# Performance work log

Hardware: AMD Instinct MI355X
Metric: run time of the kernel (lower is better)

The kernel has to match this reference:

```python
import jax, jax.numpy as jnp
import numpy as np

B, L, D, H = 2, 2048, 1024, 16
HD = D // H


def setup_inputs() -> dict:
    key = jax.random.key(0)
    ks = jax.random.split(key, 12)
    s = 1.0 / np.sqrt(D)
    inp = {
        "q": jax.random.normal(ks[0], (B, L, D), jnp.float32),
        "k": jax.random.normal(ks[1], (B, L, D), jnp.float32),
        "v": jax.random.normal(ks[2], (B, L, D), jnp.float32),
        "mask": jnp.zeros((B, L), dtype=bool),  # True = masked out
        "Wq": jax.random.normal(ks[3], (D, D), jnp.float32) * s,
        "bq": jnp.zeros((D,), jnp.float32),
        "Wk": jax.random.normal(ks[4], (D, D), jnp.float32) * s,
        "bk": jnp.zeros((D,), jnp.float32),
        "Wv": jax.random.normal(ks[5], (D, D), jnp.float32) * s,
        "bv": jnp.zeros((D,), jnp.float32),
        "Wo": jax.random.normal(ks[6], (D, D), jnp.float32) * s,
        "bo": jnp.zeros((D,), jnp.float32),
    }
    return inp


def reference(q, k, v, mask, Wq, bq, Wk, bk, Wv, bv, Wo, bo):
    # linear projections (torch Linear: x @ W.T + b), split into heads: [B,H,L,HD]
    def proj(x, W, b):
        y = jnp.einsum('bld,ed->ble', x, W) + b
        return y.reshape(x.shape[0], x.shape[1], H, HD).transpose(0, 2, 1, 3)

    Q = proj(q, Wq, bq)
    K = proj(k, Wk, bk)
    V = proj(v, Wv, bv)

    scale = 1.0 / np.sqrt(HD).astype(np.float32)
    scores = jnp.einsum('bhqd,bhkd->bhqk', Q, K) * scale  # [B,H,Lq,Lk]
    # mask [B,Lk] -> broadcast over heads and query positions
    scores = jnp.where(mask[:, None, None, :], -jnp.inf, scores)
    attn = jax.nn.softmax(scores, axis=-1)
    out = jnp.einsum('bhqk,bhkd->bhqd', attn, V)  # [B,H,Lq,HD]
    out = out.transpose(0, 2, 1, 3).reshape(q.shape[0], q.shape[1], D)
    return jnp.einsum('bld,ed->ble', out, Wo) + bo
```

## Files before the change

kernel.cpp:

```cpp
#include <hip/hip_runtime.h>

#define LSEQ 2048
#define DMODEL 1024
#define NHEAD 16
#define HDIM 64

typedef __attribute__((ext_vector_type(8))) short bf16x8;
typedef __attribute__((ext_vector_type(4))) float f32x4;
typedef __attribute__((ext_vector_type(16))) float f32x16;
typedef unsigned int u32;
typedef unsigned short u16;
typedef unsigned long long u64;

static __device__ __forceinline__ u16 f2bf(float x) {
    return (u16)((__builtin_bit_cast(u32, x) + 0x8000u) >> 16);
}

static __device__ __forceinline__ u32 f2bf_pk(float hi, float lo) {
    u32 a = __builtin_bit_cast(u32, hi) + 0x8000u;
    u32 b = __builtin_bit_cast(u32, lo) + 0x8000u;
#if __has_builtin(__builtin_amdgcn_perm)
    return __builtin_amdgcn_perm(a, b, 0x07060302u);
#else
    return (a & 0xFFFF0000u) | (b >> 16);
#endif
}

static __device__ __forceinline__ float bf2f(short s) {
    return __builtin_bit_cast(float, (u32)((u16)s) << 16);
}

static __device__ __forceinline__ float fast_exp2(float x) {
#if __has_builtin(__builtin_amdgcn_exp2f)
    return __builtin_amdgcn_exp2f(x);
#else
    return __expf(x * 0.6931471805599453f);
#endif
}

static __device__ __forceinline__ void gll16(const void* g, void* l) {
    __builtin_amdgcn_global_load_lds(
        (const __attribute__((address_space(1))) u32*)g,
        (__attribute__((address_space(3))) u32*)l, 16, 0, 0);
}

template <int N>
static __device__ __forceinline__ void vwait() {
    asm volatile("s_waitcnt vmcnt(%0)" :: "n"(N) : "memory");
}

__global__ __launch_bounds__(256) void conv_all(
    const float* __restrict__ q, const float* __restrict__ k, const float* __restrict__ v,
    const float* __restrict__ w0, const float* __restrict__ w1,
    const float* __restrict__ w2, const float* __restrict__ w3,
    u16* __restrict__ Qf, u16* __restrict__ Kf, u16* __restrict__ Vf,
    u16* __restrict__ o0, u16* __restrict__ o1, u16* __restrict__ o2,
    u16* __restrict__ o3) {
    const int bid = blockIdx.x;
    const float* s; u16* d; int off;
    if (bid < 12288) {
        const int z = bid >> 12;
        off = bid & 4095;
        if (z == 0)      { s = q; d = Qf; }
        else if (z == 1) { s = k; d = Kf; }
        else             { s = v; d = Vf; }
    } else {
        const int t = bid - 12288;
        const int z = t >> 10;
        off = t & 1023;
        if (z == 0)      { s = w0; d = o0; }
        else if (z == 1) { s = w1; d = o1; }
        else if (z == 2) { s = w2; d = o2; }
        else             { s = w3; d = o3; }
    }
    const int i = (off * 256 + threadIdx.x) * 4;
    float4 x = *(const float4*)(s + i);
    uint2 r;
    r.x = f2bf_pk(x.y, x.x);
    r.y = f2bf_pk(x.w, x.z);
    *(uint2*)(d + i) = r;
}

template <int OUT_MODE, int BN>
__device__ __forceinline__ void mfma_gemm(u16* __restrict__ sm,
                                          const u16* __restrict__ Xb,
                                          const u16* __restrict__ Wb,
                                          const float* __restrict__ bias,
                                          void* __restrict__ Yv, float scale) {
    constexpr int NB = BN / 32;
    constexpr int LPT = (BN == 128) ? 4 : 3;
    constexpr int ASZ = 4096;
    constexpr int BSZ = BN * 32;
    constexpr int NT = DMODEL / 32;
    u16* As = sm;
    u16* Bs = sm + 3 * ASZ;

    const int tid = threadIdx.x;
    const int wave = tid >> 6, lane = tid & 63;
    const int l16 = lane & 15, quad = lane >> 4;
    const int wm = (wave >> 1) * 64, wn = (wave & 1) * (BN / 2);
    const int m0 = blockIdx.x * 128, n0 = blockIdx.y * BN;

    const u16* Xr = Xb + (size_t)(m0 + (tid >> 2)) * DMODEL + (tid & 3) * 8;
    const u16* Wr = Wb + (size_t)(n0 + (tid >> 2)) * DMODEL + (tid & 3) * 8;
    const int t8 = tid * 8;

    auto stage = [&](int kt, int slot) {
        const int k0 = kt * 32;
        u16* Ab = As + slot * ASZ;
        u16* Bb = Bs + slot * BSZ;
        gll16(Xr + k0, Ab + t8);
        gll16(Xr + (size_t)64 * DMODEL + k0, Ab + 2048 + t8);
        gll16(Wr + k0, Bb + t8);
        if (BN == 128)
            gll16(Wr + (size_t)64 * DMODEL + k0, Bb + 2048 + t8);
    };

    f32x4 acc[4][NB];
    #pragma unroll
    for (int i = 0; i < 4; ++i)
        #pragma unroll
        for (int j = 0; j < NB; ++j)
            #pragma unroll
            for (int r = 0; r < 4; ++r) acc[i][j][r] = 0.0f;

    auto compute = [&](int kt) {
        const u16* Ac = As + (kt % 3) * ASZ;
        const u16* Bc = Bs + (kt % 3) * BSZ;
        bf16x8 af[4], bf[NB];
        #pragma unroll
        for (int mb = 0; mb < 4; ++mb)
            af[mb] = *(const bf16x8*)(Ac + (wm + mb * 16 + l16) * 32 + quad * 8);
        #pragma unroll
        for (int nb = 0; nb < NB; ++nb)
            bf[nb] = *(const bf16x8*)(Bc + (wn + nb * 16 + l16) * 32 + quad * 8);
        #pragma unroll
        for (int mb = 0; mb < 4; ++mb)
            #pragma unroll
            for (int nb = 0; nb < NB; ++nb)
                acc[mb][nb] = __builtin_amdgcn_mfma_f32_16x16x32_bf16(
                    af[mb], bf[nb], acc[mb][nb], 0, 0, 0);
    };

    stage(0, 0);
    stage(1, 1);

    #pragma unroll 1
    for (int kt = 0; kt < NT - 1; ++kt) {
        vwait<LPT>();
        __builtin_amdgcn_s_barrier();
        if (kt + 2 < NT) stage(kt + 2, (kt + 2) % 3);
        compute(kt);
    }
    vwait<0>();
    __builtin_amdgcn_s_barrier();
    compute(NT - 1);

    #pragma unroll
    for (int nb = 0; nb < NB; ++nb) {
        const int n = n0 + wn + nb * 16 + l16;
        const float bn = bias[n];
        #pragma unroll
        for (int mb = 0; mb < 4; ++mb) {
            const int mb0 = m0 + wm + mb * 16 + quad * 4;
            if (OUT_MODE == 2) {
                u16* Y = (u16*)Yv;
                uint2 rr;
                rr.x = f2bf_pk((acc[mb][nb][1] + bn) * scale, (acc[mb][nb][0] + bn) * scale);
                rr.y = f2bf_pk((acc[mb][nb][3] + bn) * scale, (acc[mb][nb][2] + bn) * scale);
                const int bb = mb0 >> 11, l = mb0 & 2047;
                const int h = n >> 6, hd = n & 63;
                *(uint2*)(Y + ((size_t)((bb * NHEAD + h) * HDIM) + hd) * LSEQ + l) = rr;
            } else {
                #pragma unroll
                for (int r = 0; r < 4; ++r) {
                    const int m = mb0 + r;
                    const float val = (acc[mb][nb][r] + bn) * scale;
                    if (OUT_MODE == 0) {
                        u16* Y = (u16*)Yv;
                        const int bb = m >> 11, l = m & 2047;
                        const int h = n >> 6, hd = n & 63;
                        Y[(((size_t)(bb * NHEAD + h) * LSEQ + l) * HDIM) + hd] = f2bf(val);
                    } else {
                        float* Y = (float*)Yv;
                        Y[(size_t)m * DMODEL + n] = val;
                    }
                }
            }
        }
    }
}

#define QSCALE (0.125f * 1.4426950408889634f)

__global__ __launch_bounds__(256) void qkv_gemm(
    const u16* __restrict__ Qf, const u16* __restrict__ Kf, const u16* __restrict__ Vf,
    const u16* __restrict__ Wqb, const u16* __restrict__ Wkb, const u16* __restrict__ Wvb,
    const float* __restrict__ bq, const float* __restrict__ bk, const float* __restrict__ bv,
    u16* __restrict__ Qp, u16* __restrict__ Kp, u16* __restrict__ Vtp) {
    __shared__ alignas(16) u16 sm[24576];
    if (blockIdx.z == 0)      mfma_gemm<0, 128>(sm, Qf, Wqb, bq, (void*)Qp, QSCALE);
    else if (blockIdx.z == 1) mfma_gemm<0, 128>(sm, Kf, Wkb, bk, (void*)Kp, 1.0f);
    else                      mfma_gemm<2, 128>(sm, Vf, Wvb, bv, (void*)Vtp, 1.0f);
}

__global__ __launch_bounds__(256) void out_gemm(
    const u16* __restrict__ AOb, const u16* __restrict__ Wob,
    const float* __restrict__ bo, float* __restrict__ out) {
    __shared__ alignas(16) u16 sm[18432];
    mfma_gemm<1, 64>(sm, AOb, Wob, bo, (void*)out, 1.0f);
}

#define KT 128
#define NTILE (LSEQ / KT)
#define HTILE (NTILE / 2)

__global__ __launch_bounds__(512, 2) void attn_mfma(
    const u16* __restrict__ Qp, const u16* __restrict__ Kp,
    const u16* __restrict__ Vtp, const unsigned char* __restrict__ mask,
    u16* __restrict__ P0, u16* __restrict__ P1, float* __restrict__ lbuf) {
    __shared__ alignas(16) u16 smem[32768];

    const int tid = threadIdx.x;
    const int wave = tid >> 6;
    const int lane = tid & 63;
    const int l32 = lane & 31;
    const int half = lane >> 5;
    const int bh = blockIdx.x;
    const int b = bh >> 4;
    const int h = bh & 15;
    const int q0 = blockIdx.y * 256;
    const int qw = q0 + wave * 32;
    const int z = blockIdx.z;
    const int kt0 = z * HTILE, kt1 = kt0 + HTILE;

    u16* Pz = z ? P1 : P0;
    float* lb = lbuf + z * (32 * LSEQ);

    const u16* Qg = Qp + ((size_t)bh * LSEQ + qw) * HDIM;
    const u16* Kg = Kp + (size_t)bh * LSEQ * HDIM;
    const u16* Vtg = Vtp + (size_t)bh * HDIM * LSEQ;
    const unsigned char* mg = mask + (size_t)b * LSEQ;

    bf16x8 qf[4];
    #pragma unroll
    for (int dc = 0; dc < 4; ++dc)
        qf[dc] = *(const bf16x8*)(Qg + (size_t)l32 * HDIM + dc * 16 + half * 8);

    f32x16 o0 = {}, o1 = {};
    const f32x16 zc = {};
    float ls[4] = {0.0f, 0.0f, 0.0f, 0.0f};

    auto stageK = [&](int ktile, int slot) {
        const int k0 = ktile * KT;
        u16* Kb = smem + slot * 8192;
        #pragma unroll
        for (int j = 0; j < 2; ++j) {
            const int cid = j * 512 + tid;
            const int key = cid >> 3, pc = cid & 7, c = pc ^ (key & 7);
            gll16(Kg + (size_t)(k0 + key) * HDIM + c * 8, Kb + cid * 8);
        }
    };
    auto stageV = [&](int ktile, int slot) {
        const int k0 = ktile * KT;
        u16* Vb = smem + 16384 + slot * 8192;
        #pragma unroll
        for (int j = 0; j < 2; ++j) {
            const int cid = j * 512 + tid;
            const int d = cid >> 4, pc = cid & 15, c = pc ^ (d & 15);
            gll16(Vtg + (size_t)d * LSEQ + k0 + c * 8, Vb + cid * 8);
        }
    };

    stageK(kt0, kt0 & 1); stageV(kt0, kt0 & 1);

    const u64* mg8 = (const u64*)mg;
    const u64 mm = mg8[lane] | mg8[lane + 64] | mg8[lane + 128] | mg8[lane + 192];
    const bool mask_any = __any((int)(mm != 0ULL));

    __syncthreads();

    for (int kt = kt0; kt < kt1; ++kt) {
        if (kt + 1 < kt1) {
            stageK(kt + 1, (kt + 1) & 1);
            stageV(kt + 1, (kt + 1) & 1);
        }
        const u16* Kb = smem + (kt & 1) * 8192;
        const u16* Vb = smem + 16384 + (kt & 1) * 8192;

        f32x16 st[4];
        #pragma unroll
        for (int kb = 0; kb < 4; ++kb) {
            const int key = kb * 32 + l32;
            const int phys = half ^ (key & 7);
            bf16x8 kf = *(const bf16x8*)(Kb + key * 64 + phys * 8);
            st[kb] = __builtin_amdgcn_mfma_f32_32x32x16_bf16(kf, qf[0], zc, 0, 0, 0);
        }
        #pragma unroll
        for (int dc = 1; dc < 4; ++dc)
            #pragma unroll
            for (int kb = 0; kb < 4; ++kb) {
                const int key = kb * 32 + l32;
                const int phys = (dc * 2 + half) ^ (key & 7);
                bf16x8 kf = *(const bf16x8*)(Kb + key * 64 + phys * 8);
                st[kb] = __builtin_amdgcn_mfma_f32_32x32x16_bf16(kf, qf[dc], st[kb], 0, 0, 0);
            }

        if (mask_any) {
            const int k0 = kt * KT;
            const int mb0 = mg[k0 + lane];
            const int mb1 = mg[k0 + 64 + lane];
            const float b0f = mb0 ? -1e30f : 0.0f;
            const float b1f = mb1 ? -1e30f : 0.0f;
            #pragma unroll
            for (int kb = 0; kb < 4; ++kb)
                #pragma unroll
                for (int r = 0; r < 16; ++r) {
                    const int key = kb * 32 + (r & 3) + 8 * (r >> 2) + 4 * half;
                    const float bv = __shfl((kb < 2) ? b0f : b1f, key & 63, 64);
                    st[kb][r] += bv;
                }
        }

        u32 pkn[4][8], pk[4][8];
        #pragma unroll
        for (int kb = 0; kb < 4; ++kb)
            #pragma unroll
            for (int w = 0; w < 8; ++w) {
                const float plo = fast_exp2(st[kb][2 * w]);
                const float phi = fast_exp2(st[kb][2 * w + 1]);
                ls[kb] += plo + phi;
                pkn[kb][w] = f2bf_pk(phi, plo);
            }
        #pragma unroll
        for (int kb = 0; kb < 4; ++kb)
            #pragma unroll
            for (int wb = 0; wb < 8; wb += 4) {
#if __has_builtin(__builtin_amdgcn_permlane32_swap)
                auto r02 = __builtin_amdgcn_permlane32_swap(
                    (int)pkn[kb][wb],     (int)pkn[kb][wb + 2], false, false);
                auto r13 = __builtin_amdgcn_permlane32_swap(
                    (int)pkn[kb][wb + 1], (int)pkn[kb][wb + 3], false, false);
                pk[kb][wb]     = (u32)r02[0]; pk[kb][wb + 2] = (u32)r02[1];
                pk[kb][wb + 1] = (u32)r13[0]; pk[kb][wb + 3] = (u32)r13[1];
#else
                const u32 ta = half ? pkn[kb][wb] : pkn[kb][wb + 2];
                const u32 tb = half ? pkn[kb][wb + 1] : pkn[kb][wb + 3];
                const u32 xa = __shfl_xor((int)ta, 32, 64);
                const u32 xb = __shfl_xor((int)tb, 32, 64);
                pk[kb][wb]     = half ? xa : pkn[kb][wb];
                pk[kb][wb + 1] = half ? xb : pkn[kb][wb + 1];
                pk[kb][wb + 2] = half ? pkn[kb][wb + 2] : xa;
                pk[kb][wb + 3] = half ? pkn[kb][wb + 3] : xb;
#endif
            }

        #pragma unroll
        for (int c = 0; c < 8; ++c) {
            const int kb = c >> 1, wb = 4 * (c & 1);
            bf16x8 pb = __builtin_bit_cast(bf16x8, *(uint4*)&pk[kb][wb]);
            {
                const int d = l32;
                const int phys = (c * 2 + half) ^ (d & 15);
                bf16x8 va = *(const bf16x8*)(Vb + d * 128 + phys * 8);
                o0 = __builtin_amdgcn_mfma_f32_32x32x16_bf16(va, pb, o0, 0, 0, 0);
            }
            {
                const int d = 32 + l32;
                const int phys = (c * 2 + half) ^ (d & 15);
                bf16x8 va = *(const bf16x8*)(Vb + d * 128 + phys * 8);
                o1 = __builtin_amdgcn_mfma_f32_32x32x16_bf16(va, pb, o1, 0, 0, 0);
            }
        }

        __syncthreads();
    }

    const float l_l = (ls[0] + ls[1]) + (ls[2] + ls[3]);
    const float l_tot = l_l + __shfl_xor(l_l, 32, 64);
    if (!half) lb[bh * LSEQ + qw + l32] = l_tot;
    __syncthreads();
    u16* T = smem;
    #pragma unroll
    for (int nb = 0; nb < 2; ++nb)
        #pragma unroll
        for (int rp = 0; rp < 8; ++rp) {
            const int r = rp * 2;
            const int d = nb * 32 + (r & 3) + 8 * (r >> 2) + 4 * half;
            const float vlo = (nb ? o1[r] : o0[r]);
            const float vhi = (nb ? o1[r + 1] : o0[r + 1]);
            *(u32*)(T + (wave * 32 + l32) * 72 + d) = f2bf_pk(vhi, vlo);
        }
    __syncthreads();
    #pragma unroll
    for (int i = 0; i < 4; ++i) {
        const int cid = i * 512 + tid;
        const int row = cid >> 3, ch = cid & 7;
        bf16x8 val = *(const bf16x8*)(T + row * 72 + ch * 8);
        *(bf16x8*)(Pz + ((size_t)(b * LSEQ + q0 + row) * DMODEL) + h * HDIM + ch * 8) = val;
    }
}

__global__ __launch_bounds__(256) void combine(
    const u16* __restrict__ P0, const u16* __restrict__ P1,
    const float* __restrict__ lbuf, u16* __restrict__ AOb) {
    const int c = (blockIdx.x * 256 + threadIdx.x) * 8;
    const int bl = c >> 10;
    const int k = c & 1023;
    const int h = k >> 6;
    const int b = bl >> 11, l = bl & 2047;
    const int li = ((b << 4) + h) * LSEQ + l;
    const float inv = 1.0f / (lbuf[li] + lbuf[32 * LSEQ + li]);
    bf16x8 x0 = *(const bf16x8*)(P0 + c);
    bf16x8 x1 = *(const bf16x8*)(P1 + c);
    u32 r[4];
    #pragma unroll
    for (int j = 0; j < 4; ++j) {
        const float lo = (bf2f(x0[2 * j]) + bf2f(x1[2 * j])) * inv;
        const float hi = (bf2f(x0[2 * j + 1]) + bf2f(x1[2 * j + 1])) * inv;
        r[j] = f2bf_pk(hi, lo);
    }
    *(uint4*)(AOb + c) = *(uint4*)r;
}

extern "C" void kernel_launch(void* const* d_in, const int* in_sizes, int n_in,
                              void* d_out, int out_size, void* d_ws, size_t ws_size,
                              hipStream_t stream) {
    (void)in_sizes; (void)n_in; (void)out_size; (void)ws_size;
    const float* q  = (const float*)d_in[0];
    const float* k  = (const float*)d_in[1];
    const float* v  = (const float*)d_in[2];
    const unsigned char* mask = (const unsigned char*)d_in[3];
    const float* Wq = (const float*)d_in[4];
    const float* bq = (const float*)d_in[5];
    const float* Wk = (const float*)d_in[6];
    const float* bk = (const float*)d_in[7];
    const float* Wv = (const float*)d_in[8];
    const float* bv = (const float*)d_in[9];
    const float* Wo = (const float*)d_in[10];
    const float* bo = (const float*)d_in[11];
    float* out = (float*)d_out;

    u16* ws16 = (u16*)d_ws;
    const size_t M4 = (size_t)4 * 1024 * 1024;
    const size_t M1 = (size_t)1024 * 1024;
    u16* Qf  = ws16;
    u16* Kf  = ws16 + M4;
    u16* Vf  = ws16 + 2 * M4;
    u16* Qp  = ws16 + 3 * M4;
    u16* Kp  = ws16 + 4 * M4;
    u16* Vtp = ws16 + 5 * M4;
    u16* AOb = ws16 + 6 * M4;
    u16* Wqb = ws16 + 7 * M4;
    u16* Wkb = ws16 + 7 * M4 + M1;
    u16* Wvb = ws16 + 7 * M4 + 2 * M1;
    u16* Wob = ws16 + 7 * M4 + 3 * M1;

    u16* P0 = Qf;
    u16* P1 = Kf;
    float* lbuf = (float*)Vf;

    conv_all<<<dim3(16384), 256, 0, stream>>>(q, k, v, Wq, Wk, Wv, Wo,
                                              Qf, Kf, Vf, Wqb, Wkb, Wvb, Wob);
    qkv_gemm<<<dim3(32, 8, 3), 256, 0, stream>>>(Qf, Kf, Vf, Wqb, Wkb, Wvb,
                                                 bq, bk, bv, Qp, Kp, Vtp);
    attn_mfma<<<dim3(32, 8, 2), 512, 0, stream>>>(Qp, Kp, Vtp, mask, P0, P1, lbuf);
    combine<<<dim3(2048), 256, 0, stream>>>(P0, P1, lbuf, AOb);
    out_gemm<<<dim3(32, 16), 256, 0, stream>>>(AOb, Wob, bo, out);
}
```

Measured before the change: 216.2 us.

## Process score sub-blocks one at a time in attention to cut registers

Restructures the per-tile attention loop so each 32-key sub-block runs QK^T, masking, exp, the lane swap and PV before the next one starts, in a non-unrolled loop. This replaces the four live score accumulators and packed-P arrays with one of each. It also raises the launch-bounds minimum from 2 to 4 blocks per CU, to push register use down and allow more resident waves. In exchange, the MFMA work of different sub-blocks can no longer be interleaved, which may expose MFMA dependency latency. Shared memory use (64KB per block) may still prevent reaching 4 blocks per CU.

```diff
diff --git a/kernel.cpp b/kernel.cpp
--- a/kernel.cpp
+++ b/kernel.cpp
@@ -215,7 +215,7 @@
 #define NTILE (LSEQ / KT)
 #define HTILE (NTILE / 2)
 
-__global__ __launch_bounds__(512, 2) void attn_mfma(
+__global__ __launch_bounds__(512, 4) void attn_mfma(
     const u16* __restrict__ Qp, const u16* __restrict__ Kp,
     const u16* __restrict__ Vtp, const unsigned char* __restrict__ mask,
     u16* __restrict__ P0, u16* __restrict__ P1, float* __restrict__ lbuf) {
@@ -248,8 +248,7 @@
         qf[dc] = *(const bf16x8*)(Qg + (size_t)l32 * HDIM + dc * 16 + half * 8);
 
     f32x16 o0 = {}, o1 = {};
-    const f32x16 zc = {};
-    float ls[4] = {0.0f, 0.0f, 0.0f, 0.0f};
+    float lsum = 0.0f;
 
     auto stageK = [&](int ktile, int slot) {
         const int k0 = ktile * KT;
@@ -288,96 +287,86 @@
         const u16* Kb = smem + (kt & 1) * 8192;
         const u16* Vb = smem + 16384 + (kt & 1) * 8192;
 
-        f32x16 st[4];
-        #pragma unroll
+        #pragma unroll 1
         for (int kb = 0; kb < 4; ++kb) {
-            const int key = kb * 32 + l32;
-            const int phys = half ^ (key & 7);
-            bf16x8 kf = *(const bf16x8*)(Kb + key * 64 + phys * 8);
-            st[kb] = __builtin_amdgcn_mfma_f32_32x32x16_bf16(kf, qf[0], zc, 0, 0, 0);
-        }
-        #pragma unroll
-        for (int dc = 1; dc < 4; ++dc)
-            #pragma unroll
-            for (int kb = 0; kb < 4; ++kb) {
+            f32x16 st = {};
+            #pragma unroll
+            for (int dc = 0; dc < 4; ++dc) {
                 const int key = kb * 32 + l32;
                 const int phys = (dc * 2 + half) ^ (key & 7);
                 bf16x8 kf = *(const bf16x8*)(Kb + key * 64 + phys * 8);
-                st[kb] = __builtin_amdgcn_mfma_f32_32x32x16_bf16(kf, qf[dc], st[kb], 0, 0, 0);
-            }
-
-        if (mask_any) {
-            const int k0 = kt * KT;
-            const int mb0 = mg[k0 + lane];
-            const int mb1 = mg[k0 + 64 + lane];
-            const float b0f = mb0 ? -1e30f : 0.0f;
-            const float b1f = mb1 ? -1e30f : 0.0f;
-            #pragma unroll
-            for (int kb = 0; kb < 4; ++kb)
+                st = __builtin_amdgcn_mfma_f32_32x32x16_bf16(kf, qf[dc], st, 0, 0, 0);
+            }
+
+            if (mask_any) {
+                const int k0 = kt * KT;
+                const int mb0 = mg[k0 + lane];
+                const int mb1 = mg[k0 + 64 + lane];
+                const float b0f = mb0 ? -1e30f : 0.0f;
+                const float b1f = mb1 ? -1e30f : 0.0f;
                 #pragma unroll
                 for (int r = 0; r < 16; ++r) {
                     const int key = kb * 32 + (r & 3) + 8 * (r >> 2) + 4 * half;
                     const float bv = __shfl((kb < 2) ? b0f : b1f, key & 63, 64);
-                    st[kb][r] += bv;
+                    st[r] += bv;
                 }
-        }
-
-        u32 pkn[4][8], pk[4][8];
-        #pragma unroll
-        for (int kb = 0; kb < 4; ++kb)
+            }
+
+            u32 pk[8];
+            float lk0 = 0.0f, lk1 = 0.0f;
             #pragma unroll
             for (int w = 0; w < 8; ++w) {
-                const float plo = fast_exp2(st[kb][2 * w]);
-                const float phi = fast_exp2(st[kb][2 * w + 1]);
-                ls[kb] += plo + phi;
-                pkn[kb][w] = f2bf_pk(phi, plo);
-            }
-        #pragma unroll
-        for (int kb = 0; kb < 4; ++kb)
+                const float plo = fast_exp2(st[2 * w]);
+                const float phi = fast_exp2(st[2 * w + 1]);
+                lk0 += plo; lk1 += phi;
+                pk[w] = f2bf_pk(phi, plo);
+            }
+            lsum += lk0 + lk1;
+
             #pragma unroll
             for (int wb = 0; wb < 8; wb += 4) {
 #if __has_builtin(__builtin_amdgcn_permlane32_swap)
                 auto r02 = __builtin_amdgcn_permlane32_swap(
-                    (int)pkn[kb][wb],     (int)pkn[kb][wb + 2], false, false);
+                    (int)pk[wb],     (int)pk[wb + 2], false, false);
                 auto r13 = __builtin_amdgcn_permlane32_swap(
-                    (int)pkn[kb][wb + 1], (int)pkn[kb][wb + 3], false, false);
-                pk[kb][wb]     = (u32)r02[0]; pk[kb][wb + 2] = (u32)r02[1];
-                pk[kb][wb + 1] = (u32)r13[0]; pk[kb][wb + 3] = (u32)r13[1];
+                    (int)pk[wb + 1], (int)pk[wb + 3], false, false);
+                pk[wb]     = (u32)r02[0]; pk[wb + 2] = (u32)r02[1];
+                pk[wb + 1] = (u32)r13[0]; pk[wb + 3] = (u32)r13[1];
 #else
-                const u32 ta = half ? pkn[kb][wb] : pkn[kb][wb + 2];
-                const u32 tb = half ? pkn[kb][wb + 1] : pkn[kb][wb + 3];
+                const u32 ta = half ? pk[wb] : pk[wb + 2];
+                const u32 tb = half ? pk[wb + 1] : pk[wb + 3];
                 const u32 xa = __shfl_xor((int)ta, 32, 64);
                 const u32 xb = __shfl_xor((int)tb, 32, 64);
-                pk[kb][wb]     = half ? xa : pkn[kb][wb];
-                pk[kb][wb + 1] = half ? xb : pkn[kb][wb + 1];
-                pk[kb][wb + 2] = half ? pkn[kb][wb + 2] : xa;
-                pk[kb][wb + 3] = half ? pkn[kb][wb + 3] : xb;
+                pk[wb]     = half ? xa : pk[wb];
+                pk[wb + 1] = half ? xb : pk[wb + 1];
+                pk[wb + 2] = half ? pk[wb + 2] : xa;
+                pk[wb + 3] = half ? pk[wb + 3] : xb;
 #endif
             }
 
-        #pragma unroll
-        for (int c = 0; c < 8; ++c) {
-            const int kb = c >> 1, wb = 4 * (c & 1);
-            bf16x8 pb = __builtin_bit_cast(bf16x8, *(uint4*)&pk[kb][wb]);
-            {
-                const int d = l32;
-                const int phys = (c * 2 + half) ^ (d & 15);
-                bf16x8 va = *(const bf16x8*)(Vb + d * 128 + phys * 8);
-                o0 = __builtin_amdgcn_mfma_f32_32x32x16_bf16(va, pb, o0, 0, 0, 0);
-            }
-            {
-                const int d = 32 + l32;
-                const int phys = (c * 2 + half) ^ (d & 15);
-                bf16x8 va = *(const bf16x8*)(Vb + d * 128 + phys * 8);
-                o1 = __builtin_amdgcn_mfma_f32_32x32x16_bf16(va, pb, o1, 0, 0, 0);
+            #pragma unroll
+            for (int cc = 0; cc < 2; ++cc) {
+                const int c = 2 * kb + cc;
+                bf16x8 pb = __builtin_bit_cast(bf16x8, *(uint4*)&pk[4 * cc]);
+                {
+                    const int d = l32;
+                    const int phys = (c * 2 + half) ^ (d & 15);
+                    bf16x8 va = *(const bf16x8*)(Vb + d * 128 + phys * 8);
+                    o0 = __builtin_amdgcn_mfma_f32_32x32x16_bf16(va, pb, o0, 0, 0, 0);
+                }
+                {
+                    const int d = 32 + l32;
+                    const int phys = (c * 2 + half) ^ (d & 15);
+                    bf16x8 va = *(const bf16x8*)(Vb + d * 128 + phys * 8);
+                    o1 = __builtin_amdgcn_mfma_f32_32x32x16_bf16(va, pb, o1, 0, 0, 0);
+                }
             }
         }
 
         __syncthreads();
     }
 
-    const float l_l = (ls[0] + ls[1]) + (ls[2] + ls[3]);
-    const float l_tot = l_l + __shfl_xor(l_l, 32, 64);
+    const float l_tot = lsum + __shfl_xor(lsum, 32, 64);
     if (!half) lb[bh * LSEQ + qw + l32] = l_tot;
     __syncthreads();
     u16* T = smem;
```

Result: no change. 216.2 us (+0.0%).
